# Performance work log

Hardware: AMD Instinct MI355X
Metric: run time of the kernel (lower is better)

## Reference

```python
import jax, jax.numpy as jnp
import numpy as np
import math

BATCH, NODES, IN_DIM = 8, 2048, 64
HEADS, OUT_DIM = 4, 32
D = HEADS * OUT_DIM
N_NEIGHBORS = 32


def setup_inputs() -> dict:
    key = jax.random.key(0)
    ks = jax.random.split(key, 6)
    s = lambda fan: 1.0 / np.sqrt(fan)
    return {
        "x": jax.random.normal(ks[0], (BATCH, NODES, IN_DIM), jnp.float32),
        "Wq": jax.random.normal(ks[1], (D, IN_DIM), jnp.float32) * s(IN_DIM),
        "bq": jnp.zeros((D,), jnp.float32),
        "Wk": jax.random.normal(ks[2], (D, IN_DIM), jnp.float32) * s(IN_DIM),
        "bk": jnp.zeros((D,), jnp.float32),
        "mlp_w": jax.random.normal(ks[3], (HEADS, HEADS), jnp.float32) * s(HEADS),
        "mlp_b": jnp.zeros((HEADS,), jnp.float32),
        "ln_g": jnp.ones((NODES,), jnp.float32),
        "ln_b": jnp.zeros((NODES,), jnp.float32),
    }


def _layernorm(x, g, b, eps=1e-5):
    m = x.mean(-1, keepdims=True)
    v = x.var(-1, keepdims=True)
    return (x - m) * jax.lax.rsqrt(v + eps) * g + b


def _forward(x, Wq, bq, Wk, bk, mlp_w, mlp_b, ln_g, ln_b):
    B, N, _ = x.shape
    # static graph branch (computed in the original forward, but its result is
    # never used in the returned adjacency -- kept for fidelity; DCE'd under jit)
    adj_static = jax.nn.softmax(
        jax.nn.relu(_layernorm(jnp.einsum('bnc,bmc->bnm', x, x), ln_g, ln_b)), axis=1)
    del adj_static

    q = x @ Wq.T + bq  # (B,N,D)
    k = x @ Wk.T + bk
    # (B,D,N) -> (B,H,d,N)
    q = q.transpose(0, 2, 1).reshape(B, HEADS, OUT_DIM, N)
    k = k.transpose(0, 2, 1).reshape(B, HEADS, OUT_DIM, N)
    q = q.transpose(0, 1, 3, 2)  # (B,H,N,d)

    # torch.split(query, chunk, dim=-1) splits q over out_dim, k over nodes; zip
    # truncates to the shorter list -> only min(nq,nk) chunks are processed.
    chunk = math.ceil(N / 2)
    nq = math.ceil(OUT_DIM / chunk)
    nk = math.ceil(N / chunk)
    inv_sqrt_d = jnp.float32(1.0 / math.sqrt(OUT_DIM))
    outs = []
    for i in range(min(nq, nk)):
        qc = q[..., i * chunk:(i + 1) * chunk]          # (B,H,N,dc)
        kc = k[..., i * chunk:(i + 1) * chunk]          # (B,H,d,Uc)
        a = jnp.einsum('bhnd,bhdu->bhnu', qc, kc) * inv_sqrt_d
        # dropout is identity in eval mode; soft-threshold with beta=0
        a = jnp.sign(a) * jax.nn.relu(jnp.abs(a))
        # 1x1 conv over head channels + relu, residual add
        a = jax.nn.relu(jnp.einsum('oh,bhnu->bonu', mlp_w, a)
                        + mlp_b[None, :, None, None]) + a
        outs.append(a)
    attn = jnp.concatenate(outs, axis=-1)               # (B,H,N,U)

    scores = attn.sum(axis=1)                           # (B,N,U)
    vals, idx = jax.lax.top_k(scores, N_NEIGHBORS)      # sorted, largest
    adj = jnp.zeros((B, N, N), x.dtype)
    bi = jnp.arange(B)[:, None, None]
    ni = jnp.arange(N)[None, :, None]
    return adj.at[bi, ni, idx].add(vals)


def reference(x, Wq, bq, Wk, bk, mlp_w, mlp_b, ln_g, ln_b):
    return _forward(x, Wq, bq, Wk, bk, mlp_w, mlp_b, ln_g, ln_b)
```

## Files before the change

### kernel.cpp

```cpp
#include <hip/hip_runtime.h>
#include <cstdint>
#include <cstddef>

#define BATCH 8
#define NODES 2048
#define IN_DIM 64
#define DTOT 128
#define NKEY 1024
#define LDK 136

typedef _Float16 half8v __attribute__((ext_vector_type(8)));
typedef _Float16 half4v __attribute__((ext_vector_type(4)));
typedef float float4v __attribute__((ext_vector_type(4)));

__device__ __forceinline__ unsigned long long shfl_xor_u64(unsigned long long x, int mask) {
    int lo = (int)(unsigned)(x & 0xffffffffull);
    int hi = (int)(unsigned)(x >> 32);
    lo = __shfl_xor(lo, mask, 64);
    hi = __shfl_xor(hi, mask, 64);
    return ((unsigned long long)(unsigned)hi << 32) | (unsigned)lo;
}

__device__ __forceinline__ unsigned long long make_key(float v, int idx) {
    unsigned u = __float_as_uint(v);
    u = (u & 0x80000000u) ? ~u : (u | 0x80000000u);
    return ((unsigned long long)u << 32) | (unsigned)(1023 - idx);
}

__global__ __launch_bounds__(256) void proj_qk(
    const float* __restrict__ x, const float* __restrict__ Wq, const float* __restrict__ bq,
    const float* __restrict__ Wk, const float* __restrict__ bk,
    float* __restrict__ qws, float* __restrict__ kws)
{
    __shared__ float xs[64 * 68];
    __shared__ float wsh[64 * 68];

    const int t = threadIdx.x;
    const int blk = blockIdx.x;
    const int b = blk / 96;
    const int idx = blk - b * 96;

    const float* W; const float* bias; float* out;
    int nbase, cbase; size_t orow;
    if (idx < 64) {
        int nt = idx >> 1, ct = idx & 1;
        nbase = nt * 64; cbase = ct * 64;
        W = Wq; bias = bq; out = qws;
        orow = (size_t)(b * NODES + nbase);
    } else {
        int i2 = idx - 64;
        int nt = i2 >> 1, ct = i2 & 1;
        nbase = nt * 64; cbase = ct * 64;
        W = Wk; bias = bk; out = kws;
        orow = (size_t)(b * NKEY + nbase);
    }

    #pragma unroll
    for (int rep = 0; rep < 4; ++rep) {
        int f = rep * 256 + t;
        int r = f >> 4, d4 = f & 15;
        float4 xv = *(const float4*)(x + ((size_t)(b * NODES + nbase + r)) * IN_DIM + d4 * 4);
        *(float4*)(xs + r * 68 + d4 * 4) = xv;
        float4 wv = *(const float4*)(W + (size_t)(cbase + r) * IN_DIM + d4 * 4);
        *(float4*)(wsh + r * 68 + d4 * 4) = wv;
    }
    __syncthreads();

    const int w = t >> 6, l = t & 63;
    const int n_sel = w * 4 + (l >> 4);
    const int ul = l & 15;

    float acc[4][4];
    #pragma unroll
    for (int i = 0; i < 4; ++i)
        #pragma unroll
        for (int j = 0; j < 4; ++j) acc[i][j] = 0.f;

    #pragma unroll
    for (int d4 = 0; d4 < 16; ++d4) {
        float4 xv[4], wv[4];
        #pragma unroll
        for (int i = 0; i < 4; ++i)
            xv[i] = *(const float4*)(xs + (n_sel * 4 + i) * 68 + d4 * 4);
        #pragma unroll
        for (int j = 0; j < 4; ++j)
            wv[j] = *(const float4*)(wsh + (j * 16 + ul) * 68 + d4 * 4);
        #pragma unroll
        for (int i = 0; i < 4; ++i)
            #pragma unroll
            for (int j = 0; j < 4; ++j)
                acc[i][j] += xv[i].x * wv[j].x + xv[i].y * wv[j].y +
                             xv[i].z * wv[j].z + xv[i].w * wv[j].w;
    }

    #pragma unroll
    for (int j = 0; j < 4; ++j) {
        float bv = bias[cbase + j * 16 + ul];
        #pragma unroll
        for (int i = 0; i < 4; ++i)
            out[(orow + n_sel * 4 + i) * DTOT + cbase + j * 16 + ul] = acc[i][j] + bv;
    }
}

__global__ __launch_bounds__(256, 2) void scores_mfma(
    const float* __restrict__ qws, const float* __restrict__ kws,
    const float* __restrict__ mlpw, const float* __restrict__ mlpb,
    float* __restrict__ adj)
{
    __shared__ _Float16 khs[64 * LDK];
    __shared__ _Float16 kls[64 * LDK];

    const int t = threadIdx.x;
    const int blk = blockIdx.x;
    const int b = blk >> 9;
    const int rem = blk & 511;
    const int nb = (rem >> 4) * 64;
    const int ub = (rem & 15) * 64;

    const int w = t >> 6, l = t & 63;
    const int quad = l >> 4, lane16 = l & 15;

    const int arow = b * NODES + nb + w * 16 + lane16;
    half8v Ah[4], Al[4];
    #pragma unroll
    for (int h = 0; h < 4; ++h) {
        const float* qp = qws + (size_t)arow * DTOT + h * 32 + quad * 8;
        float4 f0 = *(const float4*)(qp);
        float4 f1 = *(const float4*)(qp + 4);
        float tmp[8] = {f0.x, f0.y, f0.z, f0.w, f1.x, f1.y, f1.z, f1.w};
        #pragma unroll
        for (int e = 0; e < 8; ++e) {
            _Float16 hi = (_Float16)tmp[e];
            Ah[h][e] = hi;
            Al[h][e] = (_Float16)(tmp[e] - (float)hi);
        }
    }

    #pragma unroll
    for (int rep = 0; rep < 8; ++rep) {
        int f = rep * 256 + t;
        int r = f >> 5, c = f & 31;
        float4 v = *(const float4*)(kws + ((size_t)(b * NKEY + ub + r)) * DTOT + c * 4);
        float tmp[4] = {v.x, v.y, v.z, v.w};
        half4v h4, l4;
        #pragma unroll
        for (int e = 0; e < 4; ++e) {
            _Float16 hi = (_Float16)tmp[e];
            h4[e] = hi;
            l4[e] = (_Float16)(tmp[e] - (float)hi);
        }
        *(half4v*)(&khs[r * LDK + c * 4]) = h4;
        *(half4v*)(&kls[r * LDK + c * 4]) = l4;
    }
    __syncthreads();

    float mw[4][4], mb4[4];
    #pragma unroll
    for (int o = 0; o < 4; ++o) {
        mb4[o] = mlpb[o];
        #pragma unroll
        for (int h = 0; h < 4; ++h) mw[o][h] = mlpw[o * 4 + h];
    }
    const float INV = 0.17677669529663687f;

    #pragma unroll
    for (int ut = 0; ut < 4; ++ut) {
        half8v Bh[4], Bl[4];
        #pragma unroll
        for (int h = 0; h < 4; ++h) {
            Bh[h] = *(const half8v*)(&khs[(ut * 16 + lane16) * LDK + h * 32 + quad * 8]);
            Bl[h] = *(const half8v*)(&kls[(ut * 16 + lane16) * LDK + h * 32 + quad * 8]);
        }
        float4v C[4];
        #pragma unroll
        for (int h = 0; h < 4; ++h) {
            float4v c = {0.f, 0.f, 0.f, 0.f};
            c = __builtin_amdgcn_mfma_f32_16x16x32_f16(Ah[h], Bh[h], c, 0, 0, 0);
            c = __builtin_amdgcn_mfma_f32_16x16x32_f16(Ah[h], Bl[h], c, 0, 0, 0);
            c = __builtin_amdgcn_mfma_f32_16x16x32_f16(Al[h], Bh[h], c, 0, 0, 0);
            c = __builtin_amdgcn_mfma_f32_16x16x32_f16(Al[h], Bl[h], c, 0, 0, 0);
            C[h] = c;
        }
        #pragma unroll
        for (int r = 0; r < 4; ++r) {
            float a0 = C[0][r] * INV, a1 = C[1][r] * INV;
            float a2 = C[2][r] * INV, a3 = C[3][r] * INV;
            float ssum = a0 + a1 + a2 + a3;
            #pragma unroll
            for (int o = 0; o < 4; ++o) {
                float to = mw[o][0] * a0 + mw[o][1] * a1 + mw[o][2] * a2 + mw[o][3] * a3 + mb4[o];
                ssum += fmaxf(to, 0.f);
            }
            const size_t rowp = ((size_t)(b * NODES + nb + w * 16 + quad * 4 + r)) * NODES + NKEY;
            adj[rowp + ub + ut * 16 + lane16] = ssum;
        }
    }
}

__global__ __launch_bounds__(256) void topk_write(float* __restrict__ adj)
{
    __shared__ float scrow[4][1024];
    __shared__ unsigned long long cand[4][64];

    const int t = threadIdx.x;
    const int blk = blockIdx.x;
    const int b = blk >> 9;
    const int r0 = (blk & 511) * 4;
    const int w = t >> 6, l = t & 63;

    const int n = r0 + w;
    float* rowptr = adj + ((size_t)(b * NODES + n)) * NODES;
    const float* S = rowptr + NKEY;

    float v[16];
    #pragma unroll
    for (int jj = 0; jj < 16; ++jj) v[jj] = S[l + (jj << 6)];

    float lm = v[0];
    #pragma unroll
    for (int jj = 1; jj < 16; ++jj) lm = fmaxf(lm, v[jj]);

    float s = lm;
    #pragma unroll
    for (int k = 2; k <= 64; k <<= 1) {
        #pragma unroll
        for (int j = k >> 1; j > 0; j >>= 1) {
            float o = __shfl_xor(s, j, 64);
            bool up = ((l & k) == 0);
            bool lower = ((l & j) == 0);
            float mx = fmaxf(s, o), mn = fminf(s, o);
            s = (up == lower) ? mx : mn;
        }
    }
    const float T0 = __shfl(s, 31, 64);

    cand[w][l] = 0ull;
    __builtin_amdgcn_wave_barrier();
    int total = 0;
    #pragma unroll
    for (int jj = 0; jj < 16; ++jj) {
        bool p = (v[jj] >= T0);
        unsigned long long m = __ballot(p);
        if (p) {
            int pos = total + __popcll(m & ((1ull << l) - 1ull));
            if (pos < 64) cand[w][pos] = make_key(v[jj], l + (jj << 6));
        }
        total += (int)__popcll(m);
    }
    __builtin_amdgcn_wave_barrier();

    unsigned long long key;
    if (total <= 64) {
        key = cand[w][l];
        #pragma unroll
        for (int k = 2; k <= 64; k <<= 1) {
            #pragma unroll
            for (int j = k >> 1; j > 0; j >>= 1) {
                unsigned long long o = shfl_xor_u64(key, j);
                bool up = ((l & k) == 0);
                bool lower = ((l & j) == 0);
                unsigned long long mx = key > o ? key : o;
                unsigned long long mn = key > o ? o : key;
                key = (up == lower) ? mx : mn;
            }
        }
    } else {
        float selv = 0.f; int seli = 0;
        #pragma unroll 1
        for (int it = 0; it < 32; ++it) {
            float bv = -3.4e38f; int bi = 0x7fffffff;
            #pragma unroll
            for (int jj = 0; jj < 16; ++jj) {
                int idx = l + (jj << 6);
                if (v[jj] > bv) { bv = v[jj]; bi = idx; }
            }
            #pragma unroll
            for (int off = 1; off < 64; off <<= 1) {
                float ov = __shfl_xor(bv, off, 64);
                int oi = __shfl_xor(bi, off, 64);
                if (ov > bv || (ov == bv && oi < bi)) { bv = ov; bi = oi; }
            }
            if (l == it) { selv = bv; seli = bi; }
            if ((bi & 63) == l) {
                int slot = bi >> 6;
                #pragma unroll
                for (int jj = 0; jj < 16; ++jj) if (jj == slot) v[jj] = -3.4e38f;
            }
        }
        key = (l < 32) ? make_key(selv, seli) : 0ull;
    }

    __builtin_amdgcn_wave_barrier();
    #pragma unroll
    for (int jj = 0; jj < 16; ++jj) scrow[w][l + (jj << 6)] = 0.f;
    __builtin_amdgcn_wave_barrier();
    if (l < 32) {
        unsigned hi = (unsigned)(key >> 32);
        float val = __uint_as_float((hi & 0x80000000u) ? (hi & 0x7fffffffu) : ~hi);
        int idx = 1023 - (int)(key & 0xffffffffu);
        scrow[w][idx] = val;
    }
    __builtin_amdgcn_wave_barrier();

    #pragma unroll
    for (int jj = 0; jj < 8; ++jj) {
        int c4 = jj * 64 + l;
        float4 val;
        if (c4 < 256) val = *(const float4*)(&scrow[w][c4 * 4]);
        else          val = make_float4(0.f, 0.f, 0.f, 0.f);
        *(float4*)(rowptr + c4 * 4) = val;
    }
}

extern "C" void kernel_launch(void* const* d_in, const int* in_sizes, int n_in,
                              void* d_out, int out_size, void* d_ws, size_t ws_size,
                              hipStream_t stream) {
    const float* x    = (const float*)d_in[0];
    const float* Wq   = (const float*)d_in[1];
    const float* bq   = (const float*)d_in[2];
    const float* Wk   = (const float*)d_in[3];
    const float* bk   = (const float*)d_in[4];
    const float* mlpw = (const float*)d_in[5];
    const float* mlpb = (const float*)d_in[6];

    float* qws = (float*)d_ws;
    float* kws = qws + (size_t)BATCH * NODES * DTOT;
    float* adj = (float*)d_out;

    proj_qk<<<dim3(BATCH * 96), dim3(256), 0, stream>>>(x, Wq, bq, Wk, bk, qws, kws);
    scores_mfma<<<dim3(BATCH * 512), dim3(256), 0, stream>>>(qws, kws, mlpw, mlpb, adj);
    topk_write<<<dim3(BATCH * 512), dim3(256), 0, stream>>>(adj);
}
```

Baseline: 197.6 us.

## Precompute split-fp16 Q/K in projection, drop lo*lo MFMA, simplify top-k selection

The projection kernel now writes hi/lo fp16 halves of Q and K directly, so the scores kernel no longer converts from fp32 and loads half the bytes. The Al*Bl MFMA term is dropped, leaving three MFMAs per head, which slightly lowers precision. Occupancy is raised to 4 blocks per SM. In top-k, the bitonic sorts are replaced by rank counting through shared memory, and the scores are read as float4.

```diff
diff --git a/kernel.cpp b/kernel.cpp
--- a/kernel.cpp
+++ b/kernel.cpp
@@ -10,16 +10,7 @@
 #define LDK 136
 
 typedef _Float16 half8v __attribute__((ext_vector_type(8)));
-typedef _Float16 half4v __attribute__((ext_vector_type(4)));
 typedef float float4v __attribute__((ext_vector_type(4)));
-
-__device__ __forceinline__ unsigned long long shfl_xor_u64(unsigned long long x, int mask) {
-    int lo = (int)(unsigned)(x & 0xffffffffull);
-    int hi = (int)(unsigned)(x >> 32);
-    lo = __shfl_xor(lo, mask, 64);
-    hi = __shfl_xor(hi, mask, 64);
-    return ((unsigned long long)(unsigned)hi << 32) | (unsigned)lo;
-}
 
 __device__ __forceinline__ unsigned long long make_key(float v, int idx) {
     unsigned u = __float_as_uint(v);
@@ -30,7 +21,8 @@
 __global__ __launch_bounds__(256) void proj_qk(
     const float* __restrict__ x, const float* __restrict__ Wq, const float* __restrict__ bq,
     const float* __restrict__ Wk, const float* __restrict__ bk,
-    float* __restrict__ qws, float* __restrict__ kws)
+    _Float16* __restrict__ qh, _Float16* __restrict__ ql,
+    _Float16* __restrict__ kh, _Float16* __restrict__ kl)
 {
     __shared__ float xs[64 * 68];
     __shared__ float wsh[64 * 68];
@@ -40,18 +32,19 @@
     const int b = blk / 96;
     const int idx = blk - b * 96;
 
-    const float* W; const float* bias; float* out;
+    const float* W; const float* bias;
+    _Float16* oh; _Float16* ol;
     int nbase, cbase; size_t orow;
     if (idx < 64) {
         int nt = idx >> 1, ct = idx & 1;
         nbase = nt * 64; cbase = ct * 64;
-        W = Wq; bias = bq; out = qws;
+        W = Wq; bias = bq; oh = qh; ol = ql;
         orow = (size_t)(b * NODES + nbase);
     } else {
         int i2 = idx - 64;
         int nt = i2 >> 1, ct = i2 & 1;
         nbase = nt * 64; cbase = ct * 64;
-        W = Wk; bias = bk; out = kws;
+        W = Wk; bias = bk; oh = kh; ol = kl;
         orow = (size_t)(b * NKEY + nbase);
     }
 
@@ -97,13 +90,19 @@
     for (int j = 0; j < 4; ++j) {
         float bv = bias[cbase + j * 16 + ul];
         #pragma unroll
-        for (int i = 0; i < 4; ++i)
-            out[(orow + n_sel * 4 + i) * DTOT + cbase + j * 16 + ul] = acc[i][j] + bv;
-    }
-}
-
-__global__ __launch_bounds__(256, 2) void scores_mfma(
-    const float* __restrict__ qws, const float* __restrict__ kws,
+        for (int i = 0; i < 4; ++i) {
+            float a = acc[i][j] + bv;
+            _Float16 hi = (_Float16)a;
+            size_t p = (orow + n_sel * 4 + i) * DTOT + cbase + j * 16 + ul;
+            oh[p] = hi;
+            ol[p] = (_Float16)(a - (float)hi);
+        }
+    }
+}
+
+__global__ __launch_bounds__(256, 4) void scores_mfma(
+    const _Float16* __restrict__ qh, const _Float16* __restrict__ ql,
+    const _Float16* __restrict__ kh, const _Float16* __restrict__ kl,
     const float* __restrict__ mlpw, const float* __restrict__ mlpb,
     float* __restrict__ adj)
 {
@@ -120,37 +119,21 @@
     const int w = t >> 6, l = t & 63;
     const int quad = l >> 4, lane16 = l & 15;
 
-    const int arow = b * NODES + nb + w * 16 + lane16;
+    const size_t arow = (size_t)(b * NODES + nb + w * 16 + lane16);
     half8v Ah[4], Al[4];
     #pragma unroll
     for (int h = 0; h < 4; ++h) {
-        const float* qp = qws + (size_t)arow * DTOT + h * 32 + quad * 8;
-        float4 f0 = *(const float4*)(qp);
-        float4 f1 = *(const float4*)(qp + 4);
-        float tmp[8] = {f0.x, f0.y, f0.z, f0.w, f1.x, f1.y, f1.z, f1.w};
-        #pragma unroll
-        for (int e = 0; e < 8; ++e) {
-            _Float16 hi = (_Float16)tmp[e];
-            Ah[h][e] = hi;
-            Al[h][e] = (_Float16)(tmp[e] - (float)hi);
-        }
-    }
-
-    #pragma unroll
-    for (int rep = 0; rep < 8; ++rep) {
+        Ah[h] = *(const half8v*)(qh + arow * DTOT + h * 32 + quad * 8);
+        Al[h] = *(const half8v*)(ql + arow * DTOT + h * 32 + quad * 8);
+    }
+
+    #pragma unroll
+    for (int rep = 0; rep < 4; ++rep) {
         int f = rep * 256 + t;
-        int r = f >> 5, c = f & 31;
-        float4 v = *(const float4*)(kws + ((size_t)(b * NKEY + ub + r)) * DTOT + c * 4);
-        float tmp[4] = {v.x, v.y, v.z, v.w};
-        half4v h4, l4;
-        #pragma unroll
-        for (int e = 0; e < 4; ++e) {
-            _Float16 hi = (_Float16)tmp[e];
-            h4[e] = hi;
-            l4[e] = (_Float16)(tmp[e] - (float)hi);
-        }
-        *(half4v*)(&khs[r * LDK + c * 4]) = h4;
-        *(half4v*)(&kls[r * LDK + c * 4]) = l4;
+        int r = f >> 4, c = f & 15;
+        size_t src = ((size_t)(b * NKEY + ub + r)) * DTOT + c * 8;
+        *(half8v*)(&khs[r * LDK + c * 8]) = *(const half8v*)(kh + src);
+        *(half8v*)(&kls[r * LDK + c * 8]) = *(const half8v*)(kl + src);
     }
     __syncthreads();
 
@@ -178,7 +161,6 @@
             c = __builtin_amdgcn_mfma_f32_16x16x32_f16(Ah[h], Bh[h], c, 0, 0, 0);
             c = __builtin_amdgcn_mfma_f32_16x16x32_f16(Ah[h], Bl[h], c, 0, 0, 0);
             c = __builtin_amdgcn_mfma_f32_16x16x32_f16(Al[h], Bh[h], c, 0, 0, 0);
-            c = __builtin_amdgcn_mfma_f32_16x16x32_f16(Al[h], Bl[h], c, 0, 0, 0);
             C[h] = c;
         }
         #pragma unroll
@@ -201,6 +183,7 @@
 {
     __shared__ float scrow[4][1024];
     __shared__ unsigned long long cand[4][64];
+    __shared__ float maxb[4][64];
 
     const int t = threadIdx.x;
     const int blk = blockIdx.x;
@@ -210,69 +193,76 @@
 
     const int n = r0 + w;
     float* rowptr = adj + ((size_t)(b * NODES + n)) * NODES;
-    const float* S = rowptr + NKEY;
-
-    float v[16];
-    #pragma unroll
-    for (int jj = 0; jj < 16; ++jj) v[jj] = S[l + (jj << 6)];
-
-    float lm = v[0];
-    #pragma unroll
-    for (int jj = 1; jj < 16; ++jj) lm = fmaxf(lm, v[jj]);
-
-    float s = lm;
-    #pragma unroll
-    for (int k = 2; k <= 64; k <<= 1) {
-        #pragma unroll
-        for (int j = k >> 1; j > 0; j >>= 1) {
-            float o = __shfl_xor(s, j, 64);
-            bool up = ((l & k) == 0);
-            bool lower = ((l & j) == 0);
-            float mx = fmaxf(s, o), mn = fminf(s, o);
-            s = (up == lower) ? mx : mn;
-        }
-    }
-    const float T0 = __shfl(s, 31, 64);
+    const float4* S4 = (const float4*)(rowptr + NKEY);
+
+    float4 vv[4];
+    #pragma unroll
+    for (int jj = 0; jj < 4; ++jj) vv[jj] = S4[jj * 64 + l];
+
+    float m = vv[0].x;
+    #pragma unroll
+    for (int jj = 0; jj < 4; ++jj) {
+        m = fmaxf(m, vv[jj].x); m = fmaxf(m, vv[jj].y);
+        m = fmaxf(m, vv[jj].z); m = fmaxf(m, vv[jj].w);
+    }
+
+    maxb[w][l] = m;
+    __builtin_amdgcn_wave_barrier();
+    int r = 0;
+    #pragma unroll
+    for (int j = 0; j < 64; ++j) r += (maxb[w][j] > m) ? 1 : 0;
+    float sel = (r <= 31) ? m : 3.4e38f;
+    #pragma unroll
+    for (int off = 1; off < 64; off <<= 1)
+        sel = fminf(sel, __shfl_xor(sel, off, 64));
+    const float T = sel;
 
     cand[w][l] = 0ull;
     __builtin_amdgcn_wave_barrier();
     int total = 0;
     #pragma unroll
-    for (int jj = 0; jj < 16; ++jj) {
-        bool p = (v[jj] >= T0);
-        unsigned long long m = __ballot(p);
-        if (p) {
-            int pos = total + __popcll(m & ((1ull << l) - 1ull));
-            if (pos < 64) cand[w][pos] = make_key(v[jj], l + (jj << 6));
-        }
-        total += (int)__popcll(m);
-    }
-    __builtin_amdgcn_wave_barrier();
-
-    unsigned long long key;
+    for (int jj = 0; jj < 4; ++jj) {
+        #pragma unroll
+        for (int e = 0; e < 4; ++e) {
+            float v = (e == 0) ? vv[jj].x : (e == 1) ? vv[jj].y : (e == 2) ? vv[jj].z : vv[jj].w;
+            bool p = (v >= T);
+            unsigned long long msk = __ballot(p);
+            if (p) {
+                int pos = total + __popcll(msk & ((1ull << l) - 1ull));
+                if (pos < 64) cand[w][pos] = make_key(v, jj * 256 + l * 4 + e);
+            }
+            total += (int)__popcll(msk);
+        }
+    }
+    __builtin_amdgcn_wave_barrier();
+
+    bool win = false; float wval = 0.f; int widx = 0;
     if (total <= 64) {
-        key = cand[w][l];
-        #pragma unroll
-        for (int k = 2; k <= 64; k <<= 1) {
-            #pragma unroll
-            for (int j = k >> 1; j > 0; j >>= 1) {
-                unsigned long long o = shfl_xor_u64(key, j);
-                bool up = ((l & k) == 0);
-                bool lower = ((l & j) == 0);
-                unsigned long long mx = key > o ? key : o;
-                unsigned long long mn = key > o ? o : key;
-                key = (up == lower) ? mx : mn;
-            }
+        unsigned long long key = cand[w][l];
+        int r2 = 0;
+        #pragma unroll
+        for (int j = 0; j < 64; ++j) r2 += (cand[w][j] > key) ? 1 : 0;
+        if (key != 0ull && r2 < 32) {
+            win = true;
+            unsigned hi = (unsigned)(key >> 32);
+            wval = __uint_as_float((hi & 0x80000000u) ? (hi & 0x7fffffffu) : ~hi);
+            widx = 1023 - (int)(key & 0xffffffffu);
         }
     } else {
+        float vals[16];
+        #pragma unroll
+        for (int jj = 0; jj < 4; ++jj) {
+            vals[jj * 4 + 0] = vv[jj].x; vals[jj * 4 + 1] = vv[jj].y;
+            vals[jj * 4 + 2] = vv[jj].z; vals[jj * 4 + 3] = vv[jj].w;
+        }
         float selv = 0.f; int seli = 0;
         #pragma unroll 1
         for (int it = 0; it < 32; ++it) {
             float bv = -3.4e38f; int bi = 0x7fffffff;
             #pragma unroll
-            for (int jj = 0; jj < 16; ++jj) {
-                int idx = l + (jj << 6);
-                if (v[jj] > bv) { bv = v[jj]; bi = idx; }
+            for (int s = 0; s < 16; ++s) {
+                int idx = (s >> 2) * 256 + l * 4 + (s & 3);
+                if (vals[s] > bv) { bv = vals[s]; bi = idx; }
             }
             #pragma unroll
             for (int off = 1; off < 64; off <<= 1) {
@@ -281,25 +271,20 @@
                 if (ov > bv || (ov == bv && oi < bi)) { bv = ov; bi = oi; }
             }
             if (l == it) { selv = bv; seli = bi; }
-            if ((bi & 63) == l) {
-                int slot = bi >> 6;
+            if (((bi >> 2) & 63) == l) {
+                int slot = ((bi >> 8) << 2) + (bi & 3);
                 #pragma unroll
-                for (int jj = 0; jj < 16; ++jj) if (jj == slot) v[jj] = -3.4e38f;
-            }
-        }
-        key = (l < 32) ? make_key(selv, seli) : 0ull;
+                for (int s = 0; s < 16; ++s) if (s == slot) vals[s] = -3.4e38f;
+            }
+        }
+        if (l < 32) { win = true; wval = selv; widx = seli; }
     }
 
     __builtin_amdgcn_wave_barrier();
     #pragma unroll
     for (int jj = 0; jj < 16; ++jj) scrow[w][l + (jj << 6)] = 0.f;
     __builtin_amdgcn_wave_barrier();
-    if (l < 32) {
-        unsigned hi = (unsigned)(key >> 32);
-        float val = __uint_as_float((hi & 0x80000000u) ? (hi & 0x7fffffffu) : ~hi);
-        int idx = 1023 - (int)(key & 0xffffffffu);
-        scrow[w][idx] = val;
-    }
+    if (win) scrow[w][widx] = wval;
     __builtin_amdgcn_wave_barrier();
 
     #pragma unroll
@@ -323,11 +308,13 @@
     const float* mlpw = (const float*)d_in[5];
     const float* mlpb = (const float*)d_in[6];
 
-    float* qws = (float*)d_ws;
-    float* kws = qws + (size_t)BATCH * NODES * DTOT;
+    _Float16* qh = (_Float16*)d_ws;
+    _Float16* ql = qh + (size_t)BATCH * NODES * DTOT;
+    _Float16* kh = ql + (size_t)BATCH * NODES * DTOT;
+    _Float16* kl = kh + (size_t)BATCH * NKEY * DTOT;
     float* adj = (float*)d_out;
 
-    proj_qk<<<dim3(BATCH * 96), dim3(256), 0, stream>>>(x, Wq, bq, Wk, bk, qws, kws);
-    scores_mfma<<<dim3(BATCH * 512), dim3(256), 0, stream>>>(qws, kws, mlpw, mlpb, adj);
+    proj_qk<<<dim3(BATCH * 96), dim3(256), 0, stream>>>(x, Wq, bq, Wk, bk, qh, ql, kh, kl);
+    scores_mfma<<<dim3(BATCH * 512), dim3(256), 0, stream>>>(qh, ql, kh, kl, mlpw, mlpb, adj);
     topk_write<<<dim3(BATCH * 512), dim3(256), 0, stream>>>(adj);
 }
```

After: 191.1 us. 3.3% less time.
